# Optimization experiments

Measured on AMD Instinct MI355X. Metric: run time of the kernel, lower is better.

The kernel has to match this reference:

```python
import jax, jax.numpy as jnp
import numpy as np
import math

NEG = -1e9
NUM_SQUEEZE = 2


def seq_mask(lengths, max_len, dtype):
    return (jnp.arange(max_len)[None, :] < lengths[:, None]).astype(dtype)


def maximum_path(logp, attn_mask, x_lengths, y_lengths):
    """Monotonic alignment search (Viterbi DP). logp, attn_mask: [B, Tx, Ty]."""
    B, Tx, Ty = logp.shape
    logp = jnp.where(attn_mask > 0, logp, NEG)
    cols = jnp.moveaxis(logp, 2, 0)  # [Ty, B, Tx]

    v0 = jnp.where(jnp.arange(Tx)[None, :] == 0, 0.0, NEG).astype(logp.dtype)
    v0 = jnp.broadcast_to(v0, (B, Tx))

    def fwd(v, col):
        v_shift = jnp.concatenate([jnp.full((B, 1), NEG, logp.dtype), v[:, :-1]], axis=1)
        v_new = col + jnp.maximum(v, v_shift)
        return v_new, v_new

    _, values = jax.lax.scan(fwd, v0, cols)  # [Ty, B, Tx] DP table

    def bwd(index, j):
        active = j < y_lengths  # [B]
        row = jax.nn.one_hot(index, Tx, dtype=logp.dtype) * active[:, None].astype(logp.dtype)
        vprev = values[jnp.maximum(j - 1, 0)]  # [B, Tx]
        v_here = jnp.take_along_axis(vprev, index[:, None], axis=1)[:, 0]
        v_left = jnp.take_along_axis(vprev, jnp.maximum(index - 1, 0)[:, None], axis=1)[:, 0]
        dec = (index != 0) & ((index == j) | (v_here < v_left)) & active & (j > 0)
        return jnp.where(dec, index - 1, index), row

    js = jnp.arange(Ty - 1, -1, -1)
    _, rows = jax.lax.scan(bwd, x_lengths - 1, js)  # reversed j order
    path = jnp.moveaxis(jnp.flip(rows, 0), 0, 2)  # [B, Tx, Ty]
    return path * attn_mask


def setup_inputs() -> dict:
    key = jax.random.key(0)
    ks = jax.random.split(key, 6)
    B, C, Ten, Tde = 32, 80, 512, 2048
    return {
        "o_mean": jax.random.normal(ks[0], (B, C, Ten), jnp.float32),
        "o_log_scale": jax.random.normal(ks[1], (B, C, Ten), jnp.float32) * 0.1,
        "o_dur_log": jax.random.normal(ks[2], (B, 1, Ten), jnp.float32),
        "z": jax.random.normal(ks[3], (B, C, Tde), jnp.float32),
        "x_lengths": jax.random.randint(ks[4], (B,), Ten // 2, Ten + 1, jnp.int32),
        "y_lengths": jax.random.randint(ks[5], (B,), Tde // 2, Tde + 1, jnp.int32),
    }


def reference(o_mean, o_log_scale, o_dur_log, z, x_lengths, y_lengths):
    B, C, Ten = o_mean.shape
    Tde = z.shape[2]
    dt = o_mean.dtype

    # preprocess: floor y_lengths to multiple of num_squeeze
    y_lengths = (y_lengths // NUM_SQUEEZE) * NUM_SQUEEZE

    x_mask = seq_mask(x_lengths, Ten, dt)[:, None, :]   # [B,1,Tx]
    y_mask = seq_mask(y_lengths, Tde, dt)[:, None, :]   # [B,1,Ty]
    attn_mask = x_mask[:, 0, :, None] * y_mask[:, 0, None, :]  # [B,Tx,Ty]

    z = z * y_mask  # decoder output is masked

    # log-likelihood terms (torch.no_grad in original)
    o_scale = jnp.exp(-2.0 * o_log_scale)                       # [B,C,Tx]
    logp1 = jnp.sum(-0.5 * math.log(2 * math.pi) - o_log_scale, axis=1)[:, :, None]
    logp2 = jnp.einsum('bct,bcs->bts', o_scale, -0.5 * z * z)   # [B,Tx,Ty]
    logp3 = jnp.einsum('bct,bcs->bts', o_mean * o_scale, z)
    logp4 = jnp.sum(-0.5 * o_mean * o_mean * o_scale, axis=1)[:, :, None]
    logp = logp1 + logp2 + logp3 + logp4

    attn = maximum_path(logp, attn_mask, x_lengths, y_lengths)  # [B,Tx,Ty] hard path

    # compute_outputs
    y_mean = jnp.einsum('bts,bct->bcs', attn, o_mean)           # [B,C,Ty]
    y_log_scale = jnp.einsum('bts,bct->bcs', attn, o_log_scale)
    o_attn_dur = jnp.log1p(jnp.sum(attn, axis=-1))[:, None, :] * x_mask  # [B,1,Tx]

    return (
        jnp.transpose(z, (0, 2, 1)),            # z: [B,Ty,C]
        jnp.transpose(y_mean, (0, 2, 1)),       # y_mean: [B,Ty,C]
        jnp.transpose(y_log_scale, (0, 2, 1)),  # y_log_scale: [B,Ty,C]
        jnp.transpose(attn, (0, 2, 1)),         # alignments: [B,Ty,Tx]
        jnp.transpose(o_dur_log, (0, 2, 1)),    # durations_log: [B,Tx,1]
        jnp.transpose(o_attn_dur, (0, 2, 1)),   # total_durations_log: [B,Tx,1]
    )
```

## Files before the change

### kernel.cpp

```cpp
#include <hip/hip_runtime.h>
#include <math.h>

#define BB  32
#define CC  80
#define TXX 512
#define TYY 2048
#define NEGV -1e9f

typedef float v2f __attribute__((ext_vector_type(2)));

__global__ __launch_bounds__(256) void k_prep(
    const float* __restrict__ om, const float* __restrict__ ols,
    float* __restrict__ SA, float* __restrict__ SB,
    float* __restrict__ L1, float* __restrict__ L4,
    float* __restrict__ OMTf, float* __restrict__ OLSTf,
    int* __restrict__ DUR)
{
    int b = blockIdx.y;
    int t0 = blockIdx.x * 64;
    int tid = threadIdx.x;
    int cl = tid >> 6;
    int tl = tid & 63;
    __shared__ float sm[64][81], sl[64][81], ssa[64][81];
    #pragma unroll
    for (int cp = 0; cp < 20; ++cp) {
        int c = cp * 4 + cl;
        size_t gidx = ((size_t)b * CC + c) * TXX + t0 + tl;
        float m = om[gidx], ls = ols[gidx];
        float sa = expf(-2.0f * ls);
        SA[gidx] = sa;
        SB[gidx] = m * sa;
        sm[tl][c] = m; sl[tl][c] = ls; ssa[tl][c] = sa;
    }
    __syncthreads();
    if (tid < 64) {
        float l1 = 0.f, l4 = 0.f;
        #pragma unroll 4
        for (int c = 0; c < CC; ++c) {
            float m = sm[tid][c], ls = sl[tid][c], sa = ssa[tid][c];
            l1 += (-0.9189385332046727f - ls);
            l4 += ((-0.5f * m) * m) * sa;
        }
        int g = b * TXX + t0 + tid;
        L1[g] = l1; L4[g] = l4; DUR[g] = 0;
    }
    size_t obase = (size_t)b * TXX * CC + (size_t)t0 * CC;
    for (int e = tid; e < 64 * CC; e += 256) {
        int t = e / CC, c = e - t * CC;
        OMTf[obase + e]  = sm[t][c];
        OLSTf[obase + e] = sl[t][c];
    }
}

__global__ __launch_bounds__(256) void k_logp(
    const float* __restrict__ SA, const float* __restrict__ SB,
    const float* __restrict__ L1, const float* __restrict__ L4,
    const float* __restrict__ z,
    const int* __restrict__ xlp, const int* __restrict__ ylp,
    float* __restrict__ logp)
{
    int b = blockIdx.z;
    int ylen = (ylp[b] >> 1) << 1;
    int s0 = blockIdx.y * 128;
    if (s0 >= ylen) return;
    int t0 = blockIdx.x * 64;
    int xlen = xlp[b];
    int tid = threadIdx.x;

    __shared__ float sA[16][64], sB[16][64], sZ[16][128], sW[16][128];

    v2f acc2[4][4], acc3[4][4];
    #pragma unroll
    for (int i = 0; i < 4; ++i)
        #pragma unroll
        for (int p = 0; p < 4; ++p) { acc2[i][p] = (v2f){0.f, 0.f}; acc3[i][p] = (v2f){0.f, 0.f}; }

    int tt = (tid & 15) << 2;
    int ss = (tid >> 4) << 3;
    int r  = tid >> 4;
    int c4 = (tid & 15) << 2;
    int s8 = (tid & 15) << 3;

    for (int c0 = 0; c0 < CC; c0 += 16) {
        const float* pa = SA + ((size_t)b * CC + (c0 + r)) * TXX + t0 + c4;
        const float* pb = SB + ((size_t)b * CC + (c0 + r)) * TXX + t0 + c4;
        float4 va = *(const float4*)pa;
        float4 vb = *(const float4*)pb;
        *(float4*)&sA[r][c4] = va;
        *(float4*)&sB[r][c4] = vb;

        const float* pz = z + ((size_t)b * CC + (c0 + r)) * TYY + s0 + s8;
        float4 q0 = *(const float4*)pz;
        float4 q1 = *(const float4*)(pz + 4);
        float zf[8] = {q0.x, q0.y, q0.z, q0.w, q1.x, q1.y, q1.z, q1.w};
        #pragma unroll
        for (int i = 0; i < 8; ++i) {
            sZ[r][s8 + i] = zf[i];
            sW[r][s8 + i] = (-0.5f * zf[i]) * zf[i];
        }
        __syncthreads();
        #pragma unroll
        for (int kc = 0; kc < 16; ++kc) {
            float4 a2 = *(const float4*)&sA[kc][tt];
            float4 a3 = *(const float4*)&sB[kc][tt];
            const v2f* zp = (const v2f*)&sZ[kc][ss];
            const v2f* wp = (const v2f*)&sW[kc][ss];
            v2f bz[4] = {zp[0], zp[1], zp[2], zp[3]};
            v2f bw[4] = {wp[0], wp[1], wp[2], wp[3]};
            float av2[4] = {a2.x, a2.y, a2.z, a2.w};
            float av3[4] = {a3.x, a3.y, a3.z, a3.w};
            #pragma unroll
            for (int i = 0; i < 4; ++i) {
                v2f d2 = {av2[i], av2[i]};
                v2f d3 = {av3[i], av3[i]};
                #pragma unroll
                for (int p = 0; p < 4; ++p) {
                    acc2[i][p] = __builtin_elementwise_fma(d2, bw[p], acc2[i][p]);
                    acc3[i][p] = __builtin_elementwise_fma(d3, bz[p], acc3[i][p]);
                }
            }
        }
        __syncthreads();
    }

    float l1a[4], l4a[4]; int bad[4];
    #pragma unroll
    for (int i = 0; i < 4; ++i) {
        int t = t0 + tt + i;
        l1a[i] = L1[b * TXX + t];
        l4a[i] = L4[b * TXX + t];
        bad[i] = (t >= xlen);
    }
    #pragma unroll
    for (int p = 0; p < 4; ++p) {
        #pragma unroll
        for (int h = 0; h < 2; ++h) {
            int s = s0 + ss + 2 * p + h;
            float vals[4];
            #pragma unroll
            for (int i = 0; i < 4; ++i) {
                float a2v = h ? acc2[i][p].y : acc2[i][p].x;
                float a3v = h ? acc3[i][p].y : acc3[i][p].x;
                float v = ((l1a[i] + a2v) + a3v) + l4a[i];
                vals[i] = bad[i] ? NEGV : v;
            }
            float4 o; o.x = vals[0]; o.y = vals[1]; o.z = vals[2]; o.w = vals[3];
            *(float4*)&logp[((size_t)b * TYY + s) * TXX + t0 + tt] = o;
        }
    }
}

__global__ __launch_bounds__(512) void k_fwd(
    const float* __restrict__ logp, const int* __restrict__ ylp,
    unsigned long long* __restrict__ BITS64)
{
    int b = blockIdx.x;
    int tid = threadIdx.x;
    int w = tid >> 6, lane = tid & 63;
    int n = (ylp[b] >> 1) << 1;
    int nm1 = n - 1;
    int nb = (n + 63) >> 6;
    const float* lpt = logp + (size_t)b * TYY * TXX + tid;
    unsigned long long* bout = BITS64 + ((size_t)b * 8 + w) * TYY;

    __shared__ float bnd[8][4][64];

    float v = (tid == 0) ? 0.0f : NEGV;
    float c[16];
    unsigned blo = 0u, bhi = 0u;
    int rounds = nb + 7;
    for (int r = 0; r < rounds; ++r) {
        int blk = r - w;
        if (blk >= 0 && blk < nb) {
            int S0 = blk << 6;
            if (blk == 0) {
                #pragma unroll
                for (int i = 0; i < 16; ++i) c[i] = lpt[(size_t)i * TXX];
            }
            float BL;
            if (w == 0) {
                BL = NEGV;
            } else {
                const float* srcp = (lane == 0) ? &bnd[w - 1][(blk + 3) & 3][63]
                                                : &bnd[w - 1][blk & 3][lane - 1];
                BL = *srcp;
                if (blk == 0 && lane == 0) BL = NEGV;
            }
            float BLout = 0.0f;
            #pragma unroll
            for (int j = 0; j < 64; ++j) {
                float cc = c[j & 15];
                int ps = S0 + j + 16; ps = (ps > nm1) ? nm1 : ps;
                c[j & 15] = lpt[(size_t)ps * TXX];
                float left = __shfl_up(v, 1, 64);
                float blj = __uint_as_float(
                    __builtin_amdgcn_readlane(__float_as_uint(BL), j));
                if (lane == 0) left = blj;
                unsigned long long m = __ballot(v < left);
                bool me = (lane == j);
                blo = me ? (unsigned)m : blo;
                bhi = me ? (unsigned)(m >> 32) : bhi;
                v = cc + fmaxf(v, left);
                float v63 = __uint_as_float(
                    __builtin_amdgcn_readlane(__float_as_uint(v), 63));
                BLout = me ? v63 : BLout;
            }
            bnd[w][blk & 3][lane] = BLout;
            int row = S0 - 1 + lane;
            if (row >= 0 && S0 + lane < n)
                bout[row] = (((unsigned long long)bhi) << 32) | blo;
        }
        __syncthreads();
    }
}

__global__ __launch_bounds__(64) void k_bwd(
    const unsigned long long* __restrict__ BITS64, const int* __restrict__ xlp,
    const int* __restrict__ ylp, int* __restrict__ TSTAR, int* __restrict__ DUR)
{
    int b = blockIdx.x, lane = threadIdx.x;
    int ylen = (ylp[b] >> 1) << 1;
    int xlen = xlp[b];
    const unsigned long long* bb = BITS64 + (size_t)b * 8 * TYY;
    int* tst = TSTAR + b * TYY;
    int idx = xlen - 1;
    int j0 = ylen - 1;
    while (j0 >= 0) {
        int steps = (j0 + 1 < 32) ? (j0 + 1) : 32;
        int row = j0 - 1 - lane;
        int bw5 = idx >> 5; if (bw5 > 0) --bw5;
        int base_bit = bw5 << 5;
        int c0 = base_bit >> 6;
        int amt = base_bit & 63;
        unsigned long long lo = 0ull, hi = 0ull;
        if (lane < steps && row >= 0) {
            lo = bb[(size_t)c0 * TYY + row];
            if (amt) hi = bb[(size_t)(c0 + 1) * TYY + row];
        }
        unsigned long long wq = amt ? ((lo >> 32) | (hi << 32)) : lo;
        int saved = 0;
        #pragma unroll
        for (int k = 0; k < 32; ++k) {
            if (k >= steps) break;
            int j = j0 - k;
            if (lane == k) saved = idx;
            unsigned long long wk = __shfl(wq, k, 64);
            unsigned bit = (unsigned)(wk >> (idx - base_bit)) & 1u;
            int dec = (idx != 0 && j > 0 && (idx == j || bit)) ? 1 : 0;
            idx -= dec;
        }
        if (lane < steps) {
            tst[j0 - lane] = saved;
            atomicAdd(&DUR[b * TXX + saved], 1);
        }
        j0 -= steps;
    }
}

__global__ __launch_bounds__(256) void k_small(
    const float* __restrict__ odur, const int* __restrict__ xlp,
    const int* __restrict__ DUR, float* __restrict__ out4,
    float* __restrict__ out5)
{
    int gid = blockIdx.x * 256 + threadIdx.x;
    int b = gid >> 9, t = gid & 511;
    out4[gid] = odur[gid];
    int xlen = xlp[b];
    float d = (float)DUR[gid];
    out5[gid] = (t < xlen) ? log1pf(d) : 0.0f;
}

__global__ __launch_bounds__(256) void k_out_sc(
    const float* __restrict__ z, const float* __restrict__ OMTf,
    const float* __restrict__ OLSTf, const int* __restrict__ TSTAR,
    const int* __restrict__ ylp,
    float* __restrict__ out0, float* __restrict__ out1,
    float* __restrict__ out2)
{
    int b = blockIdx.y;
    int s0 = blockIdx.x * 32;
    int tid = threadIdx.x;
    int ylen = (ylp[b] >> 1) << 1;
    __shared__ int sT[32];
    __shared__ float zt[32][81];
    if (tid < 32) {
        int s = s0 + tid;
        sT[tid] = (s < ylen) ? TSTAR[b * TYY + s] : 0;
    }
    int c_l = tid >> 5, s_l = tid & 31;
    #pragma unroll
    for (int cp = 0; cp < 10; ++cp) {
        int c = cp * 8 + c_l;
        zt[s_l][c] = z[((size_t)b * CC + c) * TYY + s0 + s_l];
    }
    __syncthreads();
    for (int e = tid; e < 32 * 80; e += 256) {
        int sl = e / 80;
        int cc = e - sl * 80;
        int s = s0 + sl;
        bool valid = s < ylen;
        int t = sT[sl];
        size_t o = ((size_t)b * TYY + s) * 80 + cc;
        size_t g = ((size_t)b * TXX + t) * 80 + cc;
        out0[o] = valid ? zt[sl][cc] : 0.0f;
        out1[o] = valid ? OMTf[g]    : 0.0f;
        out2[o] = valid ? OLSTf[g]   : 0.0f;
    }
}

__global__ __launch_bounds__(256) void k_attn(
    const int* __restrict__ TSTAR, const int* __restrict__ ylp,
    float* __restrict__ out3)
{
    int b = blockIdx.y;
    int s0 = blockIdx.x * 16;
    int tid = threadIdx.x;
    int ylen = (ylp[b] >> 1) << 1;
    #pragma unroll
    for (int r = 0; r < 16; ++r) {
        int s = s0 + r;
        int tr = (s < ylen) ? TSTAR[b * TYY + s] : -1;
        int t = tid << 1;
        float2 val;
        val.x = (t == tr) ? 1.0f : 0.0f;
        val.y = (t + 1 == tr) ? 1.0f : 0.0f;
        ((float2*)(out3 + ((size_t)b * TYY + s) * TXX))[tid] = val;
    }
}

extern "C" void kernel_launch(void* const* d_in, const int* in_sizes, int n_in,
                              void* d_out, int out_size, void* d_ws, size_t ws_size,
                              hipStream_t stream)
{
    const float* om   = (const float*)d_in[0];
    const float* ols  = (const float*)d_in[1];
    const float* odur = (const float*)d_in[2];
    const float* z    = (const float*)d_in[3];
    const int* xl = (const int*)d_in[4];
    const int* yl = (const int*)d_in[5];

    float* out0 = (float*)d_out;
    float* out1 = out0 + 5242880;
    float* out2 = out0 + 10485760;
    float* out3 = out0 + 15728640;
    float* out4 = out0 + 49283072;
    float* out5 = out0 + 49299456;

    float* SA   = out0;
    float* SB   = out0 + 1310720;
    float* logp = out3;

    char* ws = (char*)d_ws;
    float* L1 = (float*)ws;
    float* L4 = (float*)(ws + 65536);
    float* OMTf  = (float*)(ws + 131072);
    float* OLSTf = (float*)(ws + 5373952);
    unsigned long long* BITS64 = (unsigned long long*)(ws + 10616832);
    int* TSTAR = (int*)(ws + 14811136);
    int* DUR   = (int*)(ws + 15073280);

    hipLaunchKernelGGL(k_prep, dim3(8, 32), dim3(256), 0, stream,
                       om, ols, SA, SB, L1, L4, OMTf, OLSTf, DUR);
    hipLaunchKernelGGL(k_logp, dim3(8, 16, 32), dim3(256), 0, stream,
                       SA, SB, L1, L4, z, xl, yl, logp);
    hipLaunchKernelGGL(k_fwd, dim3(32), dim3(512), 0, stream, logp, yl, BITS64);
    hipLaunchKernelGGL(k_bwd, dim3(32), dim3(64), 0, stream, BITS64, xl, yl, TSTAR, DUR);
    hipLaunchKernelGGL(k_small, dim3(64), dim3(256), 0, stream, odur, xl, DUR, out4, out5);
    hipLaunchKernelGGL(k_out_sc, dim3(64, 32), dim3(256), 0, stream,
                       z, OMTf, OLSTf, TSTAR, yl, out0, out1, out2);
    hipLaunchKernelGGL(k_attn, dim3(128, 32), dim3(256), 0, stream, TSTAR, yl, out3);
}
```

Before: 743.3 us.

## Widen backtrace chunks to 64 steps and derive durations by binary search

The serial backtrace kernel now handles 64 steps per chunk instead of 32. It loads two 64-bit mask words per row, covering a 128-bit window, and broadcasts them with readlane instead of shuffles, which halves the number of chunk iterations and load round-trips on the serial critical path. The per-token duration atomics are removed. k_small instead recovers each duration by binary-searching the monotone TSTAR array, which also drops the DUR zeroing in k_prep. The window must still cover the index drift within a chunk, and the search adds some work to the small kernel.

After: 669.2 us. 10.0% less time.

```diff
diff --git a/kernel.cpp b/kernel.cpp
--- a/kernel.cpp
+++ b/kernel.cpp
@@ -13,8 +13,7 @@
     const float* __restrict__ om, const float* __restrict__ ols,
     float* __restrict__ SA, float* __restrict__ SB,
     float* __restrict__ L1, float* __restrict__ L4,
-    float* __restrict__ OMTf, float* __restrict__ OLSTf,
-    int* __restrict__ DUR)
+    float* __restrict__ OMTf, float* __restrict__ OLSTf)
 {
     int b = blockIdx.y;
     int t0 = blockIdx.x * 64;
@@ -42,7 +41,7 @@
             l4 += ((-0.5f * m) * m) * sa;
         }
         int g = b * TXX + t0 + tid;
-        L1[g] = l1; L4[g] = l4; DUR[g] = 0;
+        L1[g] = l1; L4[g] = l4;
     }
     size_t obase = (size_t)b * TXX * CC + (size_t)t0 * CC;
     for (int e = tid; e < 64 * CC; e += 256) {
@@ -216,58 +215,114 @@
 
 __global__ __launch_bounds__(64) void k_bwd(
     const unsigned long long* __restrict__ BITS64, const int* __restrict__ xlp,
-    const int* __restrict__ ylp, int* __restrict__ TSTAR, int* __restrict__ DUR)
+    const int* __restrict__ ylp, int* __restrict__ TSTAR)
 {
     int b = blockIdx.x, lane = threadIdx.x;
     int ylen = (ylp[b] >> 1) << 1;
     int xlen = xlp[b];
     const unsigned long long* bb = BITS64 + (size_t)b * 8 * TYY;
     int* tst = TSTAR + b * TYY;
+
     int idx = xlen - 1;
-    int j0 = ylen - 1;
-    while (j0 >= 0) {
-        int steps = (j0 + 1 < 32) ? (j0 + 1) : 32;
-        int row = j0 - 1 - lane;
-        int bw5 = idx >> 5; if (bw5 > 0) --bw5;
-        int base_bit = bw5 << 5;
-        int c0 = base_bit >> 6;
-        int amt = base_bit & 63;
-        unsigned long long lo = 0ull, hi = 0ull;
-        if (lane < steps && row >= 0) {
-            lo = bb[(size_t)c0 * TYY + row];
-            if (amt) hi = bb[(size_t)(c0 + 1) * TYY + row];
-        }
-        unsigned long long wq = amt ? ((lo >> 32) | (hi << 32)) : lo;
-        int saved = 0;
+    int j_hi = ylen - 1;
+
+    while (j_hi >= 63) {
+        int e = idx >> 6;
+        int base_w = (e > 0) ? (e - 1) : 0;
+        int base_bit = base_w << 6;
+        int row = j_hi - 1 - lane;
+        unsigned long long wl = 0ull, wh = 0ull;
+        if (row >= 0) {
+            wl = bb[(size_t)base_w * TYY + row];
+            wh = bb[(size_t)(base_w + 1) * TYY + row];
+        }
+        unsigned wl0 = (unsigned)wl, wl1 = (unsigned)(wl >> 32);
+        unsigned wh0 = (unsigned)wh, wh1 = (unsigned)(wh >> 32);
+        int acc = 0;
+        int pos = idx - base_bit;
         #pragma unroll
-        for (int k = 0; k < 32; ++k) {
-            if (k >= steps) break;
-            int j = j0 - k;
-            if (lane == k) saved = idx;
-            unsigned long long wk = __shfl(wq, k, 64);
-            unsigned bit = (unsigned)(wk >> (idx - base_bit)) & 1u;
-            int dec = (idx != 0 && j > 0 && (idx == j || bit)) ? 1 : 0;
-            idx -= dec;
-        }
-        if (lane < steps) {
-            tst[j0 - lane] = saved;
-            atomicAdd(&DUR[b * TXX + saved], 1);
-        }
-        j0 -= steps;
-    }
+        for (int k = 0; k < 64; ++k) {
+            int j = j_hi - k;
+            unsigned a0 = __builtin_amdgcn_readlane(wl0, k);
+            unsigned a1 = __builtin_amdgcn_readlane(wl1, k);
+            unsigned c0 = __builtin_amdgcn_readlane(wh0, k);
+            unsigned c1 = __builtin_amdgcn_readlane(wh1, k);
+            unsigned long long wkl = ((unsigned long long)a1 << 32) | a0;
+            unsigned long long wkh = ((unsigned long long)c1 << 32) | c0;
+            unsigned long long sel = (pos & 64) ? wkh : wkl;
+            unsigned bit = (unsigned)(sel >> (pos & 63)) & 1u;
+            int idxv = pos + base_bit;
+            acc = (lane == k) ? idxv : acc;
+            int dec = (idxv != 0 && j > 0 && (idxv == j || bit)) ? 1 : 0;
+            pos -= dec;
+        }
+        idx = pos + base_bit;
+        tst[j_hi - lane] = acc;
+        j_hi -= 64;
+    }
+    if (j_hi >= 0) {
+        int steps = j_hi + 1;
+        int e = idx >> 6;
+        int base_w = (e > 0) ? (e - 1) : 0;
+        int base_bit = base_w << 6;
+        int row = j_hi - 1 - lane;
+        unsigned long long wl = 0ull, wh = 0ull;
+        if (row >= 0) {
+            wl = bb[(size_t)base_w * TYY + row];
+            wh = bb[(size_t)(base_w + 1) * TYY + row];
+        }
+        unsigned wl0 = (unsigned)wl, wl1 = (unsigned)(wl >> 32);
+        unsigned wh0 = (unsigned)wh, wh1 = (unsigned)(wh >> 32);
+        int acc = 0;
+        int pos = idx - base_bit;
+        for (int k = 0; k < steps; ++k) {
+            int j = j_hi - k;
+            unsigned a0 = __builtin_amdgcn_readlane(wl0, k);
+            unsigned a1 = __builtin_amdgcn_readlane(wl1, k);
+            unsigned c0 = __builtin_amdgcn_readlane(wh0, k);
+            unsigned c1 = __builtin_amdgcn_readlane(wh1, k);
+            unsigned long long wkl = ((unsigned long long)a1 << 32) | a0;
+            unsigned long long wkh = ((unsigned long long)c1 << 32) | c0;
+            unsigned long long sel = (pos & 64) ? wkh : wkl;
+            unsigned bit = (unsigned)(sel >> (pos & 63)) & 1u;
+            int idxv = pos + base_bit;
+            acc = (lane == k) ? idxv : acc;
+            int dec = (idxv != 0 && j > 0 && (idxv == j || bit)) ? 1 : 0;
+            pos -= dec;
+        }
+        if (lane < steps) tst[j_hi - lane] = acc;
+    }
+}
+
+__device__ __forceinline__ int lbound2048(const int* __restrict__ ts, int n, int x)
+{
+    int pos = 0;
+    #pragma unroll
+    for (int step = 2048; step >= 1; step >>= 1) {
+        int np = pos + step;
+        if (np <= n && ts[np - 1] < x) pos = np;
+    }
+    return pos;
 }
 
 __global__ __launch_bounds__(256) void k_small(
     const float* __restrict__ odur, const int* __restrict__ xlp,
-    const int* __restrict__ DUR, float* __restrict__ out4,
-    float* __restrict__ out5)
+    const int* __restrict__ ylp, const int* __restrict__ TSTAR,
+    float* __restrict__ out4, float* __restrict__ out5)
 {
     int gid = blockIdx.x * 256 + threadIdx.x;
     int b = gid >> 9, t = gid & 511;
     out4[gid] = odur[gid];
     int xlen = xlp[b];
-    float d = (float)DUR[gid];
-    out5[gid] = (t < xlen) ? log1pf(d) : 0.0f;
+    int ylen = (ylp[b] >> 1) << 1;
+    const int* ts = TSTAR + b * TYY;
+    float r = 0.0f;
+    if (t < xlen) {
+        int lo = lbound2048(ts, ylen, t);
+        int hi = lbound2048(ts, ylen, t + 1);
+        r = log1pf((float)(hi - lo));
+    }
+    out5[gid] = r;
 }
 
 __global__ __launch_bounds__(256) void k_out_sc(
@@ -357,15 +412,14 @@
     float* OLSTf = (float*)(ws + 5373952);
     unsigned long long* BITS64 = (unsigned long long*)(ws + 10616832);
     int* TSTAR = (int*)(ws + 14811136);
-    int* DUR   = (int*)(ws + 15073280);
 
     hipLaunchKernelGGL(k_prep, dim3(8, 32), dim3(256), 0, stream,
-                       om, ols, SA, SB, L1, L4, OMTf, OLSTf, DUR);
+                       om, ols, SA, SB, L1, L4, OMTf, OLSTf);
     hipLaunchKernelGGL(k_logp, dim3(8, 16, 32), dim3(256), 0, stream,
                        SA, SB, L1, L4, z, xl, yl, logp);
     hipLaunchKernelGGL(k_fwd, dim3(32), dim3(512), 0, stream, logp, yl, BITS64);
-    hipLaunchKernelGGL(k_bwd, dim3(32), dim3(64), 0, stream, BITS64, xl, yl, TSTAR, DUR);
-    hipLaunchKernelGGL(k_small, dim3(64), dim3(256), 0, stream, odur, xl, DUR, out4, out5);
+    hipLaunchKernelGGL(k_bwd, dim3(32), dim3(64), 0, stream, BITS64, xl, yl, TSTAR);
+    hipLaunchKernelGGL(k_small, dim3(64), dim3(256), 0, stream, odur, xl, yl, TSTAR, out4, out5);
     hipLaunchKernelGGL(k_out_sc, dim3(64, 32), dim3(256), 0, stream,
                        z, OMTf, OLSTf, TSTAR, yl, out0, out1, out2);
     hipLaunchKernelGGL(k_attn, dim3(128, 32), dim3(256), 0, stream, TSTAR, yl, out3);
```
